# Kernel optimization log

Measured on AMD Instinct MI355X. Metric: run time of the kernel, lower is better.

The kernel has to match this reference:

```python
import jax, jax.numpy as jnp
import numpy as np

NEG_SLOPE = 0.2  # PyG GATConv leaky_relu slope


def _add_self_loops(edge_index, num_nodes):
    loops = jnp.arange(num_nodes, dtype=edge_index.dtype)
    src = jnp.concatenate([edge_index[0], loops])
    dst = jnp.concatenate([edge_index[1], loops])
    return src, dst


def _gat_conv(x, src, dst, W, a_src, a_dst, b, num_nodes):
    # W: [in, H*F]; a_src, a_dst: [H, F]; b: [H*F]
    H, F = a_src.shape
    h = (x @ W).reshape(num_nodes, H, F)                # [N,H,F]
    alpha_src = jnp.einsum('nhf,hf->nh', h, a_src)      # [N,H]
    alpha_dst = jnp.einsum('nhf,hf->nh', h, a_dst)      # [N,H]
    logits = alpha_src[src] + alpha_dst[dst]            # [E,H]
    logits = jax.nn.leaky_relu(logits, NEG_SLOPE)
    # segment softmax over incoming edges of each dst node
    seg_max = jax.ops.segment_max(logits, dst, num_segments=num_nodes)  # [N,H]
    e = jnp.exp(logits - seg_max[dst])                  # [E,H]
    denom = jax.ops.segment_sum(e, dst, num_segments=num_nodes)         # [N,H]
    alpha = e / denom[dst]                              # [E,H] (self-loops guarantee denom>0)
    msg = h[src] * alpha[:, :, None]                    # [E,H,F]
    out = jax.ops.segment_sum(msg, dst, num_segments=num_nodes)         # [N,H,F]
    return out.reshape(num_nodes, H * F) + b            # concat=True


def _gcn_conv(x, src, dst, W, b, num_nodes):
    h = x @ W                                           # [N,out]
    ones = jnp.ones(dst.shape[0], dtype=h.dtype)
    deg = jax.ops.segment_sum(ones, dst, num_segments=num_nodes)        # [N]
    dinv = jnp.where(deg > 0, jax.lax.rsqrt(deg), 0.0)
    norm = dinv[src] * dinv[dst]                        # [E]
    out = jax.ops.segment_sum(h[src] * norm[:, None], dst, num_segments=num_nodes)
    return out + b


def setup_inputs() -> dict:
    key = jax.random.key(0)
    ks = jax.random.split(key, 10)
    N, E = 50000, 800000
    in_dim, hid, H1, ncls = 128, 32, 8, 16
    s = 0.05
    d = {}
    d['x'] = jax.random.normal(ks[0], (N, in_dim), jnp.float32)
    d['edge_index'] = jax.random.randint(ks[1], (2, E), 0, N)
    # GATConv 1: in=128 -> hid=32, heads=8
    d['W1'] = jax.random.normal(ks[2], (in_dim, H1 * hid), jnp.float32) * s
    d['a_src1'] = jax.random.normal(ks[3], (H1, hid), jnp.float32) * s
    d['a_dst1'] = jax.random.normal(ks[4], (H1, hid), jnp.float32) * s
    d['b1'] = jnp.zeros((H1 * hid,), jnp.float32)
    # GATConv 2: in=256 -> hid//2=16, heads=1
    d['W2'] = jax.random.normal(ks[5], (H1 * hid, hid // 2), jnp.float32) * s
    d['a_src2'] = jax.random.normal(ks[6], (1, hid // 2), jnp.float32) * s
    d['a_dst2'] = jax.random.normal(ks[7], (1, hid // 2), jnp.float32) * s
    d['b2'] = jnp.zeros((hid // 2,), jnp.float32)
    # GCNConv: 16 -> 16 classes
    d['W3'] = jax.random.normal(ks[8], (hid // 2, ncls), jnp.float32) * s
    d['b3'] = jnp.zeros((ncls,), jnp.float32)
    return d


def reference(x, edge_index, W1, a_src1, a_dst1, b1, W2, a_src2, a_dst2, b2, W3, b3):
    N = x.shape[0]
    src, dst = _add_self_loops(edge_index, N)
    # dropout layers are identity in eval mode
    h = _gat_conv(x, src, dst, W1, a_src1, a_dst1, b1, N)
    h = jax.nn.elu(h)
    h = _gat_conv(h, src, dst, W2, a_src2, a_dst2, b2, N)
    h = jax.nn.elu(h)
    out = _gcn_conv(h, src, dst, W3, b3, N)
    return out
```

## Files before the change

kernel.cpp:

```cpp
#include <hip/hip_runtime.h>
#include <hip/hip_bf16.h>
#include <math.h>

#define NEG_SLOPE 0.2f
#define DEG_CAP 64
#define FPAD 16

typedef float f32x4 __attribute__((ext_vector_type(4)));
typedef short bf16x8 __attribute__((ext_vector_type(8)));
typedef unsigned int u32x2 __attribute__((ext_vector_type(2)));

static __device__ __forceinline__ float lrelu(float x) { return x > 0.f ? x : NEG_SLOPE * x; }
static __device__ __forceinline__ float elu1(float x)  { return x > 0.f ? x : (expf(x) - 1.f); }

static __device__ __forceinline__ unsigned short f2bf(float x) {
    __hip_bfloat16 h = __float2bfloat16(x);
    return *reinterpret_cast<unsigned short*>(&h);
}
static __device__ __forceinline__ unsigned int pack2bf(float a, float b) {
    return (unsigned int)f2bf(a) | ((unsigned int)f2bf(b) << 16);
}
static __device__ __forceinline__ float bflo(unsigned int u) { return __uint_as_float(u << 16); }
static __device__ __forceinline__ float bfhi(unsigned int u) { return __uint_as_float(u & 0xFFFF0000u); }

__global__ __launch_bounds__(256) void init_kernel(int* __restrict__ fillc_p, const float* __restrict__ W1,
                                                   unsigned short* __restrict__ Wb, int N) {
    int i = blockIdx.x * 256 + threadIdx.x;
    if (i < N) fillc_p[i * FPAD] = 0;
    if (i < 32768) {
        int j = i & 7, lane = (i >> 3) & 63, t = (i >> 9) & 15, kk = i >> 13;
        int k = kk * 32 + (lane >> 4) * 8 + j;
        int n = t * 16 + (lane & 15);
        Wb[i] = f2bf(W1[k * 256 + n]);
    }
}

__global__ void fill_kernel(const int* __restrict__ ei, int* __restrict__ fillc_p,
                            int* __restrict__ srcs_p, int E, int E2) {
    int i = blockIdx.x * blockDim.x + threadIdx.x;
    if (i >= E2) return;
    int src, dst;
    if (i < E) { src = ei[i]; dst = ei[E + i]; }
    else       { src = i - E; dst = i - E; }
    int pos = atomicAdd(&fillc_p[(size_t)dst * FPAD], 1);
    if (pos < DEG_CAP) srcs_p[(size_t)dst * DEG_CAP + pos] = src;
}

__global__ __launch_bounds__(256) void gemm1_kernel(const float* __restrict__ x, const unsigned short* __restrict__ Wb,
                                                    const float* __restrict__ a_src, const float* __restrict__ a_dst,
                                                    unsigned short* __restrict__ h1b, float* __restrict__ as1,
                                                    float* __restrict__ ad1, int M) {
    int w = threadIdx.x >> 6, lane = threadIdx.x & 63;
    int quad = lane >> 4, c = lane & 15;
    int rowA = blockIdx.x * 64 + w * 16 + c;
    int rowAc = rowA < M ? rowA : M - 1;
    f32x4 acc[16];
    #pragma unroll
    for (int t = 0; t < 16; t++) acc[t] = (f32x4){0.f, 0.f, 0.f, 0.f};
    #pragma unroll
    for (int kk = 0; kk < 4; kk++) {
        const float* ap = &x[(size_t)rowAc * 128 + kk * 32 + quad * 8];
        float4 a0 = *(const float4*)ap;
        float4 a1 = *(const float4*)(ap + 4);
        union { bf16x8 v; unsigned int u[4]; } af;
        af.u[0] = pack2bf(a0.x, a0.y); af.u[1] = pack2bf(a0.z, a0.w);
        af.u[2] = pack2bf(a1.x, a1.y); af.u[3] = pack2bf(a1.z, a1.w);
        const bf16x8* bp = (const bf16x8*)&Wb[(size_t)(kk * 16) * 512 + lane * 8];
        #pragma unroll
        for (int t = 0; t < 16; t++) {
            bf16x8 bf = bp[t * 64];
            acc[t] = __builtin_amdgcn_mfma_f32_16x16x32_bf16(af.v, bf, acc[t], 0, 0, 0);
        }
    }
    int growb = blockIdx.x * 64 + w * 16 + quad * 4;
    #pragma unroll
    for (int r = 0; r < 4; r++) {
        int grow = growb + r;
        if (grow < M) {
            #pragma unroll
            for (int t = 0; t < 16; t++)
                h1b[(size_t)grow * 256 + t * 16 + c] = f2bf(acc[t][r]);
        }
    }
    float asA[8], asB[8], adA[8], adB[8];
    #pragma unroll
    for (int h = 0; h < 8; h++) {
        asA[h] = a_src[h * 32 + c];      asB[h] = a_src[h * 32 + 16 + c];
        adA[h] = a_dst[h * 32 + c];      adB[h] = a_dst[h * 32 + 16 + c];
    }
    #pragma unroll
    for (int r = 0; r < 4; r++) {
        int grow = growb + r;
        #pragma unroll
        for (int h = 0; h < 8; h++) {
            float ps = acc[2 * h][r] * asA[h] + acc[2 * h + 1][r] * asB[h];
            float pd = acc[2 * h][r] * adA[h] + acc[2 * h + 1][r] * adB[h];
            ps += __shfl_xor(ps, 1); ps += __shfl_xor(ps, 2); ps += __shfl_xor(ps, 4); ps += __shfl_xor(ps, 8);
            pd += __shfl_xor(pd, 1); pd += __shfl_xor(pd, 2); pd += __shfl_xor(pd, 4); pd += __shfl_xor(pd, 8);
            if (c == 0 && grow < M) { as1[grow * 8 + h] = ps; ad1[grow * 8 + h] = pd; }
        }
    }
}

__global__ __launch_bounds__(256) void agg1_kernel(const unsigned short* __restrict__ h1b, const float* __restrict__ asrc,
                                                   const float* __restrict__ adst, const int* __restrict__ fillc_p,
                                                   const int* __restrict__ srcs_p, const float* __restrict__ b1,
                                                   unsigned short* __restrict__ h1pb, int N) {
    int node = blockIdx.x * 4 + (threadIdx.x >> 6);
    if (node >= N) return;
    int lane = threadIdx.x & 63;
    int h = lane >> 3, e8 = lane & 7;
    float adn = adst[node * 8 + h];
    int deg = fillc_p[(size_t)node * FPAD];
    int cnt = deg < DEG_CAP ? deg : DEG_CAP;
    float4 acc = make_float4(0.f, 0.f, 0.f, 0.f);
    float den = 0.f;
    int o4 = lane * 4;
    int sv = srcs_p[node * DEG_CAP + (lane < cnt ? lane : cnt - 1)];
    int g = 0;
    for (; g + 16 <= cnt; g += 16) {
        int ssA = __shfl(sv, g + e8);
        int ssB = __shfl(sv, g + 8 + e8);
        float wA = __expf(lrelu(asrc[ssA * 8 + h] + adn));
        float wB = __expf(lrelu(asrc[ssB * 8 + h] + adn));
        uint2 v[16];
        #pragma unroll
        for (int q = 0; q < 16; q++) {
            int s = __shfl(sv, g + q);
            v[q] = *(const uint2*)&h1b[(size_t)s * 256 + o4];
        }
        #pragma unroll
        for (int q = 0; q < 8; q++) {
            float w = __shfl(wA, (h << 3) | q);
            acc.x += w * bflo(v[q].x); acc.y += w * bfhi(v[q].x);
            acc.z += w * bflo(v[q].y); acc.w += w * bfhi(v[q].y);
            den += w;
        }
        #pragma unroll
        for (int q = 8; q < 16; q++) {
            float w = __shfl(wB, (h << 3) | (q - 8));
            acc.x += w * bflo(v[q].x); acc.y += w * bfhi(v[q].x);
            acc.z += w * bflo(v[q].y); acc.w += w * bfhi(v[q].y);
            den += w;
        }
    }
    if (g + 8 <= cnt) {
        int ss = __shfl(sv, g + e8);
        float wp = __expf(lrelu(asrc[ss * 8 + h] + adn));
        uint2 v[8];
        #pragma unroll
        for (int q = 0; q < 8; q++) {
            int s = __shfl(sv, g + q);
            v[q] = *(const uint2*)&h1b[(size_t)s * 256 + o4];
        }
        #pragma unroll
        for (int q = 0; q < 8; q++) {
            float w = __shfl(wp, (h << 3) | q);
            acc.x += w * bflo(v[q].x); acc.y += w * bfhi(v[q].x);
            acc.z += w * bflo(v[q].y); acc.w += w * bfhi(v[q].y);
            den += w;
        }
        g += 8;
    }
    if (g < cnt) {
        int ep = g + e8;
        int epc = ep < cnt - 1 ? ep : cnt - 1;
        int ss = __shfl(sv, epc);
        float wp = (ep < cnt) ? __expf(lrelu(asrc[ss * 8 + h] + adn)) : 0.f;
        #pragma unroll
        for (int q = 0; q < 8; q++) {
            if (g + q < cnt) {
                int s = __shfl(sv, g + q);
                float w = __shfl(wp, (h << 3) | q);
                uint2 vv = *(const uint2*)&h1b[(size_t)s * 256 + o4];
                acc.x += w * bflo(vv.x); acc.y += w * bfhi(vv.x);
                acc.z += w * bflo(vv.y); acc.w += w * bfhi(vv.y);
                den += w;
            }
        }
    }
    float inv = 1.f / den;
    u32x2 r;
    r.x = pack2bf(elu1(acc.x * inv + b1[o4 + 0]), elu1(acc.y * inv + b1[o4 + 1]));
    r.y = pack2bf(elu1(acc.z * inv + b1[o4 + 2]), elu1(acc.w * inv + b1[o4 + 3]));
    __builtin_nontemporal_store(r, (u32x2*)&h1pb[(size_t)node * 256 + o4]);
}

__global__ __launch_bounds__(256) void gemm2_kernel(const unsigned short* __restrict__ X, const float* __restrict__ W2,
                                                    const float* __restrict__ a_src2, const float* __restrict__ a_dst2,
                                                    const int* __restrict__ fillc_p, float* __restrict__ h2,
                                                    float* __restrict__ asrc2, float* __restrict__ adst2,
                                                    float* __restrict__ dinv, int N) {
    int lane = threadIdx.x & 63;
    int c = lane & 15, kq = lane >> 4;
    int wid = blockIdx.x * (blockDim.x >> 6) + (threadIdx.x >> 6);
    int nwaves = gridDim.x * (blockDim.x >> 6);
    float w2r[64];
    #pragma unroll
    for (int i = 0; i < 64; i++) w2r[i] = W2[(kq * 64 + i) * 16 + c];
    float as_c = a_src2[c], ad_c = a_dst2[c];
    for (int n = wid; n < N; n += nwaves) {
        const unsigned short* xp = &X[(size_t)n * 256 + kq * 64];
        float acc = 0.f;
        #pragma unroll
        for (int i8 = 0; i8 < 8; i8++) {
            uint4 xv = *(const uint4*)&xp[i8 * 8];
            int b = i8 * 8;
            acc += bflo(xv.x) * w2r[b+0] + bfhi(xv.x) * w2r[b+1]
                 + bflo(xv.y) * w2r[b+2] + bfhi(xv.y) * w2r[b+3]
                 + bflo(xv.z) * w2r[b+4] + bfhi(xv.z) * w2r[b+5]
                 + bflo(xv.w) * w2r[b+6] + bfhi(xv.w) * w2r[b+7];
        }
        acc += __shfl_xor(acc, 16);
        acc += __shfl_xor(acc, 32);
        float s1 = acc * as_c, s2 = acc * ad_c;
        #pragma unroll
        for (int off = 1; off < 16; off <<= 1) { s1 += __shfl_xor(s1, off); s2 += __shfl_xor(s2, off); }
        if (kq == 0) h2[n * 16 + c] = acc;
        if (lane == 0) {
            asrc2[n] = s1; adst2[n] = s2;
            dinv[n] = rsqrtf((float)fillc_p[(size_t)n * FPAD]);
        }
    }
}

__global__ __launch_bounds__(256) void agg2_kernel(const float* __restrict__ h2, const float* __restrict__ asrc2,
                                                   const float* __restrict__ adst2, const int* __restrict__ fillc_p,
                                                   const int* __restrict__ srcs_p, const float* __restrict__ b2,
                                                   const float* __restrict__ W3, float* __restrict__ h4, int N) {
    int node = blockIdx.x * 4 + (threadIdx.x >> 6);
    if (node >= N) return;
    int lane = threadIdx.x & 63;
    int e16 = lane >> 2, seg = lane & 3;
    float adn = adst2[node];
    int deg = fillc_p[(size_t)node * FPAD];
    int cnt = deg < DEG_CAP ? deg : DEG_CAP;
    int sv = srcs_p[node * DEG_CAP + (lane < cnt ? lane : cnt - 1)];
    float wv = (lane < cnt) ? __expf(lrelu(asrc2[sv] + adn)) : 0.f;
    float4 acc = make_float4(0.f, 0.f, 0.f, 0.f);
    float den = 0.f;
    #pragma unroll
    for (int r = 0; r < 4; r++) {
        if (r * 16 < cnt) {
            int j = r * 16 + e16;
            int s = __shfl(sv, j);
            float w = __shfl(wv, j);
            const float4 v = *(const float4*)&h2[(size_t)s * 16 + seg * 4];
            acc.x += w * v.x; acc.y += w * v.y; acc.z += w * v.z; acc.w += w * v.w;
            den += w;
        }
    }
    #pragma unroll
    for (int off = 4; off < 64; off <<= 1) {
        acc.x += __shfl_xor(acc.x, off); acc.y += __shfl_xor(acc.y, off);
        acc.z += __shfl_xor(acc.z, off); acc.w += __shfl_xor(acc.w, off);
        den += __shfl_xor(den, off);
    }
    float inv = 1.f / den;
    float h3v[4];
    h3v[0] = elu1(acc.x * inv + b2[seg * 4 + 0]);
    h3v[1] = elu1(acc.y * inv + b2[seg * 4 + 1]);
    h3v[2] = elu1(acc.z * inv + b2[seg * 4 + 2]);
    h3v[3] = elu1(acc.w * inv + b2[seg * 4 + 3]);
    int c = lane & 15;
    float h4v = 0.f;
    #pragma unroll
    for (int cs = 0; cs < 16; cs++) {
        float hv = __shfl(h3v[cs & 3], cs >> 2);
        h4v += hv * W3[cs * 16 + c];
    }
    if (lane < 16) h4[node * 16 + c] = h4v;
}

__global__ __launch_bounds__(256) void agg3_kernel(const float* __restrict__ h4, const float* __restrict__ dinv,
                                                   const int* __restrict__ fillc_p, const int* __restrict__ srcs_p,
                                                   const float* __restrict__ b3, float* __restrict__ out, int N) {
    int node = blockIdx.x * 4 + (threadIdx.x >> 6);
    if (node >= N) return;
    int lane = threadIdx.x & 63;
    int e16 = lane >> 2, seg = lane & 3;
    int deg = fillc_p[(size_t)node * FPAD];
    int cnt = deg < DEG_CAP ? deg : DEG_CAP;
    int sv = srcs_p[node * DEG_CAP + (lane < cnt ? lane : cnt - 1)];
    float wv = (lane < cnt) ? dinv[sv] : 0.f;
    float4 acc = make_float4(0.f, 0.f, 0.f, 0.f);
    #pragma unroll
    for (int r = 0; r < 4; r++) {
        if (r * 16 < cnt) {
            int j = r * 16 + e16;
            int s = __shfl(sv, j);
            float w = __shfl(wv, j);
            const float4 v = *(const float4*)&h4[(size_t)s * 16 + seg * 4];
            acc.x += w * v.x; acc.y += w * v.y; acc.z += w * v.z; acc.w += w * v.w;
        }
    }
    #pragma unroll
    for (int off = 4; off < 64; off <<= 1) {
        acc.x += __shfl_xor(acc.x, off); acc.y += __shfl_xor(acc.y, off);
        acc.z += __shfl_xor(acc.z, off); acc.w += __shfl_xor(acc.w, off);
    }
    if (lane < 4) {
        float dn = dinv[node];
        float4 r;
        r.x = acc.x * dn + b3[seg * 4 + 0];
        r.y = acc.y * dn + b3[seg * 4 + 1];
        r.z = acc.z * dn + b3[seg * 4 + 2];
        r.w = acc.w * dn + b3[seg * 4 + 3];
        *(float4*)&out[(size_t)node * 16 + seg * 4] = r;
    }
}

extern "C" void kernel_launch(void* const* d_in, const int* in_sizes, int n_in,
                              void* d_out, int out_size, void* d_ws, size_t ws_size,
                              hipStream_t stream) {
    const float* x      = (const float*)d_in[0];
    const int*   ei     = (const int*)d_in[1];
    const float* W1     = (const float*)d_in[2];
    const float* a_src1 = (const float*)d_in[3];
    const float* a_dst1 = (const float*)d_in[4];
    const float* b1     = (const float*)d_in[5];
    const float* W2     = (const float*)d_in[6];
    const float* a_src2 = (const float*)d_in[7];
    const float* a_dst2 = (const float*)d_in[8];
    const float* b2     = (const float*)d_in[9];
    const float* W3     = (const float*)d_in[10];
    const float* b3     = (const float*)d_in[11];
    float* out = (float*)d_out;

    const int N  = in_sizes[0] / 128;
    const int E  = in_sizes[1] / 2;
    const int E2 = E + N;

    char* p = (char*)d_ws;
    auto alloc = [&](size_t bytes) -> void* {
        void* r = (void*)p;
        p += (bytes + 255) & ~(size_t)255;
        return r;
    };
    int*   fillc_p = (int*)alloc((size_t)N * FPAD * 4);
    int*   srcs_p  = (int*)alloc((size_t)N * DEG_CAP * 4);
    unsigned short* Wb   = (unsigned short*)alloc((size_t)32768 * 2);
    unsigned short* h1b  = (unsigned short*)alloc((size_t)N * 256 * 2);
    unsigned short* h1pb = (unsigned short*)alloc((size_t)N * 256 * 2);
    float* as1    = (float*)alloc((size_t)N * 8 * 4);
    float* ad1    = (float*)alloc((size_t)N * 8 * 4);
    float* h2     = (float*)alloc((size_t)N * 16 * 4);
    float* as2    = (float*)alloc((size_t)N * 4);
    float* ad2    = (float*)alloc((size_t)N * 4);
    float* h4     = (float*)alloc((size_t)N * 16 * 4);
    float* dinv   = (float*)alloc((size_t)N * 4);

    init_kernel<<<(N + 255) / 256, 256, 0, stream>>>(fillc_p, W1, Wb, N);
    fill_kernel<<<(E2 + 255) / 256, 256, 0, stream>>>(ei, fillc_p, srcs_p, E, E2);

    gemm1_kernel<<<(N + 63) / 64, 256, 0, stream>>>(x, Wb, a_src1, a_dst1, h1b, as1, ad1, N);
    agg1_kernel<<<(N + 3) / 4, 256, 0, stream>>>(h1b, as1, ad1, fillc_p, srcs_p, b1, h1pb, N);

    gemm2_kernel<<<1024, 256, 0, stream>>>(h1pb, W2, a_src2, a_dst2, fillc_p, h2, as2, ad2, dinv, N);
    agg2_kernel<<<(N + 3) / 4, 256, 0, stream>>>(h2, as2, ad2, fillc_p, srcs_p, b2, W3, h4, N);

    agg3_kernel<<<(N + 3) / 4, 256, 0, stream>>>(h4, dinv, fillc_p, srcs_p, b3, out, N);
}
```

Baseline: 325.4 us.

## Partition fill by destination group, split agg1 launch, batch gather loads in agg2/agg3

The fill kernel now launches eight times as many blocks, and each block handles only edges whose destination falls in one of eight residue classes. This is meant to localize atomics and scattered writes, likely to improve cache or L2 locality, at the cost of reading the edge list eight times. agg1 is split into two launches over halves of the node range. agg2 and agg3 issue all four gather loads up front without the cnt guard so they can overlap, relying on padded indices and zero weights for inactive lanes.

```diff
diff --git a/kernel.cpp b/kernel.cpp
--- a/kernel.cpp
+++ b/kernel.cpp
@@ -35,13 +35,15 @@
     }
 }
 
-__global__ void fill_kernel(const int* __restrict__ ei, int* __restrict__ fillc_p,
-                            int* __restrict__ srcs_p, int E, int E2) {
-    int i = blockIdx.x * blockDim.x + threadIdx.x;
+__global__ __launch_bounds__(256) void fill_kernel(const int* __restrict__ ei, int* __restrict__ fillc_p,
+                                                   int* __restrict__ srcs_p, int E, int E2) {
+    int g = blockIdx.x & 7;
+    int i = (blockIdx.x >> 3) * 256 + threadIdx.x;
     if (i >= E2) return;
     int src, dst;
     if (i < E) { src = ei[i]; dst = ei[E + i]; }
     else       { src = i - E; dst = i - E; }
+    if ((dst & 7) != g) return;
     int pos = atomicAdd(&fillc_p[(size_t)dst * FPAD], 1);
     if (pos < DEG_CAP) srcs_p[(size_t)dst * DEG_CAP + pos] = src;
 }
@@ -105,9 +107,9 @@
 __global__ __launch_bounds__(256) void agg1_kernel(const unsigned short* __restrict__ h1b, const float* __restrict__ asrc,
                                                    const float* __restrict__ adst, const int* __restrict__ fillc_p,
                                                    const int* __restrict__ srcs_p, const float* __restrict__ b1,
-                                                   unsigned short* __restrict__ h1pb, int N) {
-    int node = blockIdx.x * 4 + (threadIdx.x >> 6);
-    if (node >= N) return;
+                                                   unsigned short* __restrict__ h1pb, int n0, int n1) {
+    int node = n0 + blockIdx.x * 4 + (threadIdx.x >> 6);
+    if (node >= n1) return;
     int lane = threadIdx.x & 63;
     int h = lane >> 3, e8 = lane & 7;
     float adn = adst[node * 8 + h];
@@ -237,18 +239,21 @@
     int cnt = deg < DEG_CAP ? deg : DEG_CAP;
     int sv = srcs_p[node * DEG_CAP + (lane < cnt ? lane : cnt - 1)];
     float wv = (lane < cnt) ? __expf(lrelu(asrc2[sv] + adn)) : 0.f;
+    float w[4]; float4 v[4];
+    #pragma unroll
+    for (int r = 0; r < 4; r++) {
+        int j = r * 16 + e16;
+        int s = __shfl(sv, j);
+        w[r] = __shfl(wv, j);
+        v[r] = *(const float4*)&h2[(size_t)s * 16 + seg * 4];
+    }
     float4 acc = make_float4(0.f, 0.f, 0.f, 0.f);
     float den = 0.f;
     #pragma unroll
     for (int r = 0; r < 4; r++) {
-        if (r * 16 < cnt) {
-            int j = r * 16 + e16;
-            int s = __shfl(sv, j);
-            float w = __shfl(wv, j);
-            const float4 v = *(const float4*)&h2[(size_t)s * 16 + seg * 4];
-            acc.x += w * v.x; acc.y += w * v.y; acc.z += w * v.z; acc.w += w * v.w;
-            den += w;
-        }
+        acc.x += w[r] * v[r].x; acc.y += w[r] * v[r].y;
+        acc.z += w[r] * v[r].z; acc.w += w[r] * v[r].w;
+        den += w[r];
     }
     #pragma unroll
     for (int off = 4; off < 64; off <<= 1) {
@@ -283,16 +288,19 @@
     int cnt = deg < DEG_CAP ? deg : DEG_CAP;
     int sv = srcs_p[node * DEG_CAP + (lane < cnt ? lane : cnt - 1)];
     float wv = (lane < cnt) ? dinv[sv] : 0.f;
+    float w[4]; float4 v[4];
+    #pragma unroll
+    for (int r = 0; r < 4; r++) {
+        int j = r * 16 + e16;
+        int s = __shfl(sv, j);
+        w[r] = __shfl(wv, j);
+        v[r] = *(const float4*)&h4[(size_t)s * 16 + seg * 4];
+    }
     float4 acc = make_float4(0.f, 0.f, 0.f, 0.f);
     #pragma unroll
     for (int r = 0; r < 4; r++) {
-        if (r * 16 < cnt) {
-            int j = r * 16 + e16;
-            int s = __shfl(sv, j);
-            float w = __shfl(wv, j);
-            const float4 v = *(const float4*)&h4[(size_t)s * 16 + seg * 4];
-            acc.x += w * v.x; acc.y += w * v.y; acc.z += w * v.z; acc.w += w * v.w;
-        }
+        acc.x += w[r] * v[r].x; acc.y += w[r] * v[r].y;
+        acc.z += w[r] * v[r].z; acc.w += w[r] * v[r].w;
     }
     #pragma unroll
     for (int off = 4; off < 64; off <<= 1) {
@@ -351,10 +359,13 @@
     float* dinv   = (float*)alloc((size_t)N * 4);
 
     init_kernel<<<(N + 255) / 256, 256, 0, stream>>>(fillc_p, W1, Wb, N);
-    fill_kernel<<<(E2 + 255) / 256, 256, 0, stream>>>(ei, fillc_p, srcs_p, E, E2);
+    fill_kernel<<<8 * ((E2 + 255) / 256), 256, 0, stream>>>(ei, fillc_p, srcs_p, E, E2);
 
     gemm1_kernel<<<(N + 63) / 64, 256, 0, stream>>>(x, Wb, a_src1, a_dst1, h1b, as1, ad1, N);
-    agg1_kernel<<<(N + 3) / 4, 256, 0, stream>>>(h1b, as1, ad1, fillc_p, srcs_p, b1, h1pb, N);
+
+    int half = N / 2;
+    agg1_kernel<<<(half + 3) / 4, 256, 0, stream>>>(h1b, as1, ad1, fillc_p, srcs_p, b1, h1pb, 0, half);
+    agg1_kernel<<<(N - half + 3) / 4, 256, 0, stream>>>(h1b, as1, ad1, fillc_p, srcs_p, b1, h1pb, half, N);
 
     gemm2_kernel<<<1024, 256, 0, stream>>>(h1pb, W2, a_src2, a_dst2, fillc_p, h2, as2, ad2, dinv, N);
     agg2_kernel<<<(N + 3) / 4, 256, 0, stream>>>(h2, as2, ad2, fillc_p, srcs_p, b2, W3, h4, N);
```

New measurement: 309.3 us. 5.0% less time.
